# Kernel optimization log

Measured on AMD Instinct MI355X. Metric: run time of the kernel, lower is better.

## Reference

```python
import jax, jax.numpy as jnp
import numpy as np

B, T = 4096, 2048
VOCAB, E, H = 1000, 8, 8


def setup_inputs() -> dict:
    key = jax.random.key(0)
    ks = jax.random.split(key, 8)
    x = jax.random.randint(ks[0], (B, T), 0, VOCAB)
    emb = jax.random.normal(ks[1], (VOCAB, E), dtype=jnp.float32)
    s = 1.0 / np.sqrt(H)
    W_ih = jax.random.uniform(ks[2], (4 * H, E), minval=-s, maxval=s, dtype=jnp.float32)
    W_hh = jax.random.uniform(ks[3], (4 * H, H), minval=-s, maxval=s, dtype=jnp.float32)
    b_ih = jax.random.uniform(ks[4], (4 * H,), minval=-s, maxval=s, dtype=jnp.float32)
    b_hh = jax.random.uniform(ks[5], (4 * H,), minval=-s, maxval=s, dtype=jnp.float32)
    W_cls = jax.random.uniform(ks[6], (1, H), minval=-s, maxval=s, dtype=jnp.float32)
    b_cls = jax.random.uniform(ks[7], (1,), minval=-s, maxval=s, dtype=jnp.float32)
    return {"x": x, "emb": emb, "W_ih": W_ih, "W_hh": W_hh, "b_ih": b_ih,
            "b_hh": b_hh, "W_cls": W_cls, "b_cls": b_cls}


def reference(x, emb, W_ih, W_hh, b_ih, b_hh, W_cls, b_cls):
    embeds = emb[x]  # [B, T, E]
    # Precompute input contribution to all 4 gates (i, f, g, o order like PyTorch).
    xg = jnp.einsum('bte,ge->btg', embeds, W_ih) + (b_ih + b_hh)  # [B, T, 4H]

    def step(carry, xg_t):
        h, c = carry
        gates = xg_t + h @ W_hh.T  # [B, 4H]
        i, f, g, o = jnp.split(gates, 4, axis=-1)
        i = jax.nn.sigmoid(i)
        f = jax.nn.sigmoid(f)
        g = jnp.tanh(g)
        o = jax.nn.sigmoid(o)
        c = f * c + i * g
        h = o * jnp.tanh(c)
        return (h, c), None

    h0 = jnp.zeros((x.shape[0], W_hh.shape[1]), dtype=emb.dtype)
    (h_last, _), _ = jax.lax.scan(step, (h0, h0), jnp.swapaxes(xg, 0, 1))
    out = jax.nn.sigmoid(h_last @ W_cls.T + b_cls)  # [B, 1]
    return out
```

## Files before the change

kernel.cpp:

```cpp
#include <hip/hip_runtime.h>

#define TT 2048
#define NV 1000
#define LOG2E 1.4426950408889634f

__device__ __forceinline__ float tanh_fast(float x) {
    const float L = 7.90531110763549805f;
    x = __builtin_amdgcn_fmed3f(x, -L, L);
    float x2 = x * x;
    float p = -2.76076847742355e-16f;
    p = __builtin_fmaf(p, x2, 2.00018790482477e-13f);
    p = __builtin_fmaf(p, x2, -8.60467152213735e-11f);
    p = __builtin_fmaf(p, x2, 5.12229709037114e-08f);
    p = __builtin_fmaf(p, x2, 1.48572235717979e-05f);
    p = __builtin_fmaf(p, x2, 6.37261928875436e-04f);
    p = __builtin_fmaf(p, x2, 4.89352455891786e-03f);
    float q = 1.19825839466702e-06f;
    q = __builtin_fmaf(q, x2, 1.18534705686654e-04f);
    q = __builtin_fmaf(q, x2, 2.26843463243900e-03f);
    q = __builtin_fmaf(q, x2, 4.89352518554385e-03f);
    float r = __builtin_amdgcn_rcpf(q);
    return (x * p) * r;
}

template <int CTRL>
__device__ __forceinline__ float dppf(float x) {
    return __int_as_float(__builtin_amdgcn_update_dpp(
        0, __float_as_int(x), CTRL, 0xF, 0xF, true));
}
#define DPP_XOR1 0xB1
#define DPP_XOR2 0x4E
#define DPP_XOR3 0x1B
#define DPP_ROR4 0x124
#define DPP_HMIR 0x141
#define DPP_ROR8 0x128

extern "C" __global__ void __launch_bounds__(256, 1)
lstm_fused(const int* __restrict__ x, const float* __restrict__ emb,
           const float* __restrict__ W_ih, const float* __restrict__ W_hh,
           const float* __restrict__ b_ih, const float* __restrict__ b_hh,
           const float* __restrict__ W_cls, const float* __restrict__ b_cls,
           float* __restrict__ out)
{
    extern __shared__ float TAB[];

    const int tid = threadIdx.x;
    const int l   = tid & 15;
    const int s   = l >> 3;
    const int j   = l & 7;
    const int grp = tid >> 4;

    const int glo = j + (s << 4);
    const int ghi = glo + 8;
    const float scx = s ? (-2.0f * LOG2E) : -LOG2E;
    const float scy = -LOG2E;
    const float kL  = s ? 1.0f : 0.0f;
    const bool is0 = (s == 0);

    {
        float wl[8], wh[8];
        #pragma unroll
        for (int k = 0; k < 8; ++k) {
            wl[k] = W_ih[glo * 8 + k];
            wh[k] = W_ih[ghi * 8 + k];
        }
        const float bl = b_ih[glo] + b_hh[glo];
        const float bh = b_ih[ghi] + b_hh[ghi];
        for (int v = grp; v < NV; v += 16) {
            const float4 e0 = *(const float4*)(emb + v * 8);
            const float4 e1 = *(const float4*)(emb + v * 8 + 4);
            float dl = bl + e0.x*wl[0] + e0.y*wl[1] + e0.z*wl[2] + e0.w*wl[3]
                          + e1.x*wl[4] + e1.y*wl[5] + e1.z*wl[6] + e1.w*wl[7];
            float dh = bh + e0.x*wh[0] + e0.y*wh[1] + e0.z*wh[2] + e0.w*wh[3]
                          + e1.x*wh[4] + e1.y*wh[5] + e1.z*wh[6] + e1.w*wh[7];
            *(float2*)(TAB + v * 32 + l * 2) = make_float2(scx * dl, scy * dh);
        }
    }
    __syncthreads();

    const int b = blockIdx.x * 16 + grp;
    const int* __restrict__ xrow = x + (size_t)b * TT;
    const char* __restrict__ TABl = (const char*)TAB + l * 8;

    float wlo[8], whi[8];
    #pragma unroll
    for (int m = 0; m < 8; ++m) {
        wlo[m] = scx * W_hh[glo * 8 + (j ^ m)];
        whi[m] = scy * W_hh[ghi * 8 + (j ^ m)];
    }

    float c  = 0.0f;
    float hn = 0.0f;

    int4 iA = *(const int4*)(xrow);
    int4 iB = *(const int4*)(xrow + 4);
    float2 xg0 = *(const float2*)(TABl + (iA.x << 7));
    float2 xg1 = *(const float2*)(TABl + (iA.y << 7));

#define STEP(XG, NIDX) do {                                                      \
        float mm  = dppf<DPP_HMIR>(hn);                       \
        float uAl = __builtin_fmaf(wlo[0], hn, XG.x);                            \
        float uAh = __builtin_fmaf(whi[0], hn, XG.y);                            \
        float uBl = dppf<DPP_XOR1>(hn) * wlo[1];                                 \
        float uBh = dppf<DPP_XOR1>(hn) * whi[1];                                 \
        uAl = __builtin_fmaf(dppf<DPP_XOR2>(hn), wlo[2], uAl);                   \
        uAh = __builtin_fmaf(dppf<DPP_XOR2>(hn), whi[2], uAh);                   \
        uBl = __builtin_fmaf(dppf<DPP_XOR3>(hn), wlo[3], uBl);                   \
        uBh = __builtin_fmaf(dppf<DPP_XOR3>(hn), whi[3], uBh);                   \
        uAl = __builtin_fmaf(dppf<DPP_XOR3>(mm), wlo[4], uAl);                   \
        uAh = __builtin_fmaf(dppf<DPP_XOR3>(mm), whi[4], uAh);                   \
        uBl = __builtin_fmaf(dppf<DPP_XOR2>(mm), wlo[5], uBl);                   \
        uBh = __builtin_fmaf(dppf<DPP_XOR2>(mm), whi[5], uBh);                   \
        uAl = __builtin_fmaf(dppf<DPP_XOR1>(mm), wlo[6], uAl);                   \
        uAh = __builtin_fmaf(dppf<DPP_XOR1>(mm), whi[6], uAh);                   \
        uBl = __builtin_fmaf(mm, wlo[7], uBl);                                   \
        uBh = __builtin_fmaf(mm, whi[7], uBh);                                   \
        float ul = uAl + uBl;          \
        float uh = uAh + uBh;                       \
        XG = *(const float2*)(TABl + ((NIDX) << 7));           \
        float el = __builtin_amdgcn_exp2f(fminf(ul, 126.0f));                    \
        float ey = __builtin_amdgcn_exp2f(uh);                                   \
        float nl = __builtin_fmaf(-kL, el, 1.0f);           \
        float aL = nl * __builtin_amdgcn_rcpf(1.0f + el);    \
        float sy = __builtin_amdgcn_rcpf(1.0f + ey);          \
        float IG  = dppf<DPP_ROR8>(aL) * aL;           \
        float pHi = dppf<DPP_ROR8>(sy);                                          \
        float F   = is0 ? sy : pHi;                                  \
        float O   = is0 ? pHi : sy;                                  \
        c  = __builtin_fmaf(F, c, IG);                                           \
        float uc = fminf(c * (-2.0f * LOG2E), 126.0f);                           \
        float ec = __builtin_amdgcn_exp2f(uc);                                   \
        float tc = (1.0f - ec) * __builtin_amdgcn_rcpf(1.0f + ec);               \
        hn = O * tc;                                                             \
    } while (0)

    for (int t = 0; t < TT; t += 4) {
        const int nb = (t + 8 < TT) ? (t / 4 + 2) : 0;
        int4 iN = *(const int4*)(xrow + nb * 4);
        STEP(xg0, iA.z);
        STEP(xg1, iA.w);
        STEP(xg0, iB.x);
        STEP(xg1, iB.y);
        iA = iB; iB = iN;
    }
#undef STEP

    {
        float v1 = dppf<DPP_XOR1>(hn);
        float v2 = dppf<DPP_XOR2>(hn);
        float v3 = dppf<DPP_XOR3>(hn);
        float v4 = dppf<DPP_ROR4>(hn);
        float v5 = dppf<DPP_XOR1>(v4);
        float v6 = dppf<DPP_XOR2>(v4);
        float v7 = dppf<DPP_XOR3>(v4);
        if (l == 0) {
            float z = b_cls[0]
                + hn * W_cls[0] + v1 * W_cls[1] + v2 * W_cls[2] + v3 * W_cls[3]
                + v4 * W_cls[4] + v5 * W_cls[5] + v6 * W_cls[6] + v7 * W_cls[7];
            out[b] = __builtin_fmaf(0.5f, tanh_fast(0.5f * z), 0.5f);
        }
    }
}

extern "C" void kernel_launch(void* const* d_in, const int* in_sizes, int n_in,
                              void* d_out, int out_size, void* d_ws, size_t ws_size,
                              hipStream_t stream)
{
    (void)in_sizes; (void)n_in; (void)d_ws; (void)ws_size; (void)out_size;
    const int*   x     = (const int*)  d_in[0];
    const float* emb   = (const float*)d_in[1];
    const float* W_ih  = (const float*)d_in[2];
    const float* W_hh  = (const float*)d_in[3];
    const float* b_ih  = (const float*)d_in[4];
    const float* b_hh  = (const float*)d_in[5];
    const float* W_cls = (const float*)d_in[6];
    const float* b_cls = (const float*)d_in[7];
    float* out = (float*)d_out;

    const int lds_bytes = NV * 16 * 8;
    hipFuncSetAttribute((const void*)lstm_fused,
                        hipFuncAttributeMaxDynamicSharedMemorySize, lds_bytes);

    lstm_fused<<<dim3(256), dim3(256), lds_bytes, stream>>>(
        x, emb, W_ih, W_hh, b_ih, b_hh, W_cls, b_cls, out);
}
```

Baseline: 297.1 us.

## Assign one gate row per lane with 32 lanes per sequence

Each sequence is now spread over 32 lanes instead of 16, with every lane computing a single gate pre-activation rather than two. Blocks grow to 512 threads, and the table, recurrent weights and cross-lane exchange are rebuilt around a ds_swizzle xor-16 plus quad DPP permutes. The goal is a shorter per-step serial dependency chain through the recurrence, with less work per lane. In exchange there are more lanes per batch row, an extra swizzle and ROR shuffles on the critical path, and twice the thread count for the same batch.

```diff
diff --git a/kernel.cpp b/kernel.cpp
--- a/kernel.cpp
+++ b/kernel.cpp
@@ -28,14 +28,17 @@
     return __int_as_float(__builtin_amdgcn_update_dpp(
         0, __float_as_int(x), CTRL, 0xF, 0xF, true));
 }
-#define DPP_XOR1 0xB1
-#define DPP_XOR2 0x4E
-#define DPP_XOR3 0x1B
+#define DPP_QP1  0xB1
+#define DPP_QP2  0x4E
+#define DPP_QP3  0x1B
 #define DPP_ROR4 0x124
-#define DPP_HMIR 0x141
 #define DPP_ROR8 0x128
 
-extern "C" __global__ void __launch_bounds__(256, 1)
+__device__ __forceinline__ float swz_xor16(float x) {
+    return __int_as_float(__builtin_amdgcn_ds_swizzle(__float_as_int(x), 0x401F));
+}
+
+extern "C" __global__ void __launch_bounds__(512, 2)
 lstm_fused(const int* __restrict__ x, const float* __restrict__ emb,
            const float* __restrict__ W_ih, const float* __restrict__ W_hh,
            const float* __restrict__ b_ih, const float* __restrict__ b_hh,
@@ -45,93 +48,77 @@
     extern __shared__ float TAB[];
 
     const int tid = threadIdx.x;
-    const int l   = tid & 15;
-    const int s   = l >> 3;
-    const int j   = l & 7;
-    const int grp = tid >> 4;
-
-    const int glo = j + (s << 4);
-    const int ghi = glo + 8;
-    const float scx = s ? (-2.0f * LOG2E) : -LOG2E;
-    const float scy = -LOG2E;
-    const float kL  = s ? 1.0f : 0.0f;
-    const bool is0 = (s == 0);
+    const int L   = tid & 31;
+    const int grp = tid >> 5;
+    const int q   = (L >> 2) & 3;
+    const int hi  = L >> 4;
+    const int j   = (hi << 2) | (L & 3);
+    const int grow = q * 8 + j;
+    const bool isG  = (q == 2);
+    const float sc  = isG ? (-2.0f * LOG2E) : -LOG2E;
+    const float kL  = isG ? 1.0f : 0.0f;
+    const bool isq1  = (q == 1);
+    const bool isOdd = (q & 1);
 
     {
-        float wl[8], wh[8];
+        float w[8];
         #pragma unroll
-        for (int k = 0; k < 8; ++k) {
-            wl[k] = W_ih[glo * 8 + k];
-            wh[k] = W_ih[ghi * 8 + k];
-        }
-        const float bl = b_ih[glo] + b_hh[glo];
-        const float bh = b_ih[ghi] + b_hh[ghi];
+        for (int k = 0; k < 8; ++k) w[k] = W_ih[grow * 8 + k];
+        const float bb = b_ih[grow] + b_hh[grow];
         for (int v = grp; v < NV; v += 16) {
             const float4 e0 = *(const float4*)(emb + v * 8);
             const float4 e1 = *(const float4*)(emb + v * 8 + 4);
-            float dl = bl + e0.x*wl[0] + e0.y*wl[1] + e0.z*wl[2] + e0.w*wl[3]
-                          + e1.x*wl[4] + e1.y*wl[5] + e1.z*wl[6] + e1.w*wl[7];
-            float dh = bh + e0.x*wh[0] + e0.y*wh[1] + e0.z*wh[2] + e0.w*wh[3]
-                          + e1.x*wh[4] + e1.y*wh[5] + e1.z*wh[6] + e1.w*wh[7];
-            *(float2*)(TAB + v * 32 + l * 2) = make_float2(scx * dl, scy * dh);
+            float d = bb + e0.x*w[0] + e0.y*w[1] + e0.z*w[2] + e0.w*w[3]
+                         + e1.x*w[4] + e1.y*w[5] + e1.z*w[6] + e1.w*w[7];
+            TAB[v * 32 + L] = sc * d;
         }
     }
     __syncthreads();
 
     const int b = blockIdx.x * 16 + grp;
     const int* __restrict__ xrow = x + (size_t)b * TT;
-    const char* __restrict__ TABl = (const char*)TAB + l * 8;
+    const char* __restrict__ TABl = (const char*)TAB + L * 4;
 
-    float wlo[8], whi[8];
+    float w[8];
     #pragma unroll
-    for (int m = 0; m < 8; ++m) {
-        wlo[m] = scx * W_hh[glo * 8 + (j ^ m)];
-        whi[m] = scy * W_hh[ghi * 8 + (j ^ m)];
-    }
+    for (int m = 0; m < 8; ++m)
+        w[m] = sc * W_hh[grow * 8 + (j ^ m)];
 
     float c  = 0.0f;
     float hn = 0.0f;
 
     int4 iA = *(const int4*)(xrow);
     int4 iB = *(const int4*)(xrow + 4);
-    float2 xg0 = *(const float2*)(TABl + (iA.x << 7));
-    float2 xg1 = *(const float2*)(TABl + (iA.y << 7));
+    float xg0 = *(const float*)(TABl + (iA.x << 7));
+    float xg1 = *(const float*)(TABl + (iA.y << 7));
 
-#define STEP(XG, NIDX) do {                                                      \
-        float mm  = dppf<DPP_HMIR>(hn);                       \
-        float uAl = __builtin_fmaf(wlo[0], hn, XG.x);                            \
-        float uAh = __builtin_fmaf(whi[0], hn, XG.y);                            \
-        float uBl = dppf<DPP_XOR1>(hn) * wlo[1];                                 \
-        float uBh = dppf<DPP_XOR1>(hn) * whi[1];                                 \
-        uAl = __builtin_fmaf(dppf<DPP_XOR2>(hn), wlo[2], uAl);                   \
-        uAh = __builtin_fmaf(dppf<DPP_XOR2>(hn), whi[2], uAh);                   \
-        uBl = __builtin_fmaf(dppf<DPP_XOR3>(hn), wlo[3], uBl);                   \
-        uBh = __builtin_fmaf(dppf<DPP_XOR3>(hn), whi[3], uBh);                   \
-        uAl = __builtin_fmaf(dppf<DPP_XOR3>(mm), wlo[4], uAl);                   \
-        uAh = __builtin_fmaf(dppf<DPP_XOR3>(mm), whi[4], uAh);                   \
-        uBl = __builtin_fmaf(dppf<DPP_XOR2>(mm), wlo[5], uBl);                   \
-        uBh = __builtin_fmaf(dppf<DPP_XOR2>(mm), whi[5], uBh);                   \
-        uAl = __builtin_fmaf(dppf<DPP_XOR1>(mm), wlo[6], uAl);                   \
-        uAh = __builtin_fmaf(dppf<DPP_XOR1>(mm), whi[6], uAh);                   \
-        uBl = __builtin_fmaf(mm, wlo[7], uBl);                                   \
-        uBh = __builtin_fmaf(mm, whi[7], uBh);                                   \
-        float ul = uAl + uBl;          \
-        float uh = uAh + uBh;                       \
-        XG = *(const float2*)(TABl + ((NIDX) << 7));           \
-        float el = __builtin_amdgcn_exp2f(fminf(ul, 126.0f));                    \
-        float ey = __builtin_amdgcn_exp2f(uh);                                   \
-        float nl = __builtin_fmaf(-kL, el, 1.0f);           \
-        float aL = nl * __builtin_amdgcn_rcpf(1.0f + el);    \
-        float sy = __builtin_amdgcn_rcpf(1.0f + ey);          \
-        float IG  = dppf<DPP_ROR8>(aL) * aL;           \
-        float pHi = dppf<DPP_ROR8>(sy);                                          \
-        float F   = is0 ? sy : pHi;                                  \
-        float O   = is0 ? pHi : sy;                                  \
-        c  = __builtin_fmaf(F, c, IG);                                           \
-        float uc = fminf(c * (-2.0f * LOG2E), 126.0f);                           \
-        float ec = __builtin_amdgcn_exp2f(uc);                                   \
-        float tc = (1.0f - ec) * __builtin_amdgcn_rcpf(1.0f + ec);               \
-        hn = O * tc;                                                             \
+#define STEP(XG, NIDX) do {                                                    \
+        float hs = swz_xor16(hn);                   \
+        float uA = __builtin_fmaf(w[0], hn, XG);                               \
+        float uB = dppf<DPP_QP1>(hn) * w[1];                                   \
+        uA = __builtin_fmaf(dppf<DPP_QP2>(hn), w[2], uA);                      \
+        uB = __builtin_fmaf(dppf<DPP_QP3>(hn), w[3], uB);                      \
+        uA = __builtin_fmaf(hs, w[4], uA);                                     \
+        uB = __builtin_fmaf(dppf<DPP_QP1>(hs), w[5], uB);                      \
+        uA = __builtin_fmaf(dppf<DPP_QP2>(hs), w[6], uA);                      \
+        uB = __builtin_fmaf(dppf<DPP_QP3>(hs), w[7], uB);                      \
+        float u = uA + uB;                                                     \
+        XG = *(const float*)(TABl + ((NIDX) << 7));          \
+        float e  = __builtin_amdgcn_exp2f(fminf(u, 126.0f));                   \
+        float nl = __builtin_fmaf(-kL, e, 1.0f);         \
+        float a  = nl * __builtin_amdgcn_rcpf(1.0f + e);                       \
+        float ar = dppf<DPP_ROR8>(a);                        \
+        float P  = a * ar;                                    \
+        float Pr = dppf<DPP_ROR4>(P);                         \
+        float Fv = isq1 ? a  : ar;                      \
+        float Ov = isq1 ? ar : a;                       \
+        c = __builtin_fmaf(Fv, c, Pr);                                         \
+        float uc = fminf(c * (-2.0f * LOG2E), 126.0f);                         \
+        float ec = __builtin_amdgcn_exp2f(uc);                                 \
+        float tc = (1.0f - ec) * __builtin_amdgcn_rcpf(1.0f + ec);             \
+        float h  = Ov * tc;                                  \
+        float hq = dppf<DPP_ROR4>(h);                        \
+        hn = isOdd ? h : hq;                                                   \
     } while (0)
 
     for (int t = 0; t < TT; t += 4) {
@@ -146,17 +133,17 @@
 #undef STEP
 
     {
-        float v1 = dppf<DPP_XOR1>(hn);
-        float v2 = dppf<DPP_XOR2>(hn);
-        float v3 = dppf<DPP_XOR3>(hn);
-        float v4 = dppf<DPP_ROR4>(hn);
-        float v5 = dppf<DPP_XOR1>(v4);
-        float v6 = dppf<DPP_XOR2>(v4);
-        float v7 = dppf<DPP_XOR3>(v4);
-        if (l == 0) {
+        float hs = swz_xor16(hn);
+        float v1 = dppf<DPP_QP1>(hn);
+        float v2 = dppf<DPP_QP2>(hn);
+        float v3 = dppf<DPP_QP3>(hn);
+        float v5 = dppf<DPP_QP1>(hs);
+        float v6 = dppf<DPP_QP2>(hs);
+        float v7 = dppf<DPP_QP3>(hs);
+        if (L == 0) {
             float z = b_cls[0]
                 + hn * W_cls[0] + v1 * W_cls[1] + v2 * W_cls[2] + v3 * W_cls[3]
-                + v4 * W_cls[4] + v5 * W_cls[5] + v6 * W_cls[6] + v7 * W_cls[7];
+                + hs * W_cls[4] + v5 * W_cls[5] + v6 * W_cls[6] + v7 * W_cls[7];
             out[b] = __builtin_fmaf(0.5f, tanh_fast(0.5f * z), 0.5f);
         }
     }
@@ -177,10 +164,10 @@
     const float* b_cls = (const float*)d_in[7];
     float* out = (float*)d_out;
 
-    const int lds_bytes = NV * 16 * 8;
+    const int lds_bytes = NV * 32 * 4;
     hipFuncSetAttribute((const void*)lstm_fused,
                         hipFuncAttributeMaxDynamicSharedMemorySize, lds_bytes);
 
-    lstm_fused<<<dim3(256), dim3(256), lds_bytes, stream>>>(
+    lstm_fused<<<dim3(256), dim3(512), lds_bytes, stream>>>(
         x, emb, W_ih, W_hh, b_ih, b_hh, W_cls, b_cls, out);
 }
```

After: 384.0 us. +29.2%, slower.
